# Optimization experiments

Hardware: AMD Instinct MI355X
Metric: run time of the kernel (lower is better)

The kernel has to match this reference:

```python
import jax, jax.numpy as jnp
import numpy as np

B_SZ, D_MODEL, H, W = 4, 192, 64, 64
D_STATE, D_CONV, EXPAND = 16, 4, 2
D_INNER = EXPAND * D_MODEL            # 384
DT_RANK = int(np.ceil(D_MODEL / 16))  # 12


def setup_inputs() -> dict:
    key = jax.random.key(0)
    ks = jax.random.split(key, 12)
    s = 0.02
    # dt bias init so softplus(bias) lands in [1e-3, 0.1] (standard Mamba init)
    dt = jnp.exp(jax.random.uniform(ks[9], (D_INNER,)) * (np.log(0.1) - np.log(1e-3)) + np.log(1e-3))
    dt_proj_b = dt + jnp.log(-jnp.expm1(-dt))
    A_log = jnp.log(jnp.tile(jnp.arange(1, D_STATE + 1, dtype=jnp.float32), (D_INNER, 1)))
    return {
        "x": jax.random.normal(ks[0], (B_SZ, D_MODEL, H, W), jnp.float32),
        "guide": jax.random.normal(ks[1], (B_SZ, D_MODEL, H, W), jnp.float32),
        "guide_w": jax.random.normal(ks[2], (D_MODEL, D_MODEL), jnp.float32) * s,
        "ln_g": jnp.ones((D_MODEL,), jnp.float32),
        "ln_b": jnp.zeros((D_MODEL,), jnp.float32),
        "in_proj_w": jax.random.normal(ks[3], (2 * D_INNER, D_MODEL), jnp.float32) * s,
        "conv_w": jax.random.normal(ks[4], (D_INNER, D_CONV), jnp.float32) * 0.1,
        "conv_b": jnp.zeros((D_INNER,), jnp.float32),
        "x_proj_w": jax.random.normal(ks[5], (DT_RANK + 2 * D_STATE, D_INNER), jnp.float32) * s,
        "dt_proj_w": jax.random.normal(ks[6], (D_INNER, DT_RANK), jnp.float32) * s,
        "dt_proj_b": dt_proj_b,
        "A_log": A_log,
        "D": jnp.ones((D_INNER,), jnp.float32),
        "out_proj_w": jax.random.normal(ks[7], (D_MODEL, D_INNER), jnp.float32) * s,
    }


def reference(x, guide, guide_w, ln_g, ln_b, in_proj_w, conv_w, conv_b,
              x_proj_w, dt_proj_w, dt_proj_b, A_log, D, out_proj_w):
    B, C, Hh, Ww = x.shape
    L = Hh * Ww
    # 1x1 guide conv fuse, flatten to raster sequence [B, L, C]
    g = jnp.einsum('oc,bchw->bohw', guide_w, guide)
    seq = (x + g).reshape(B, C, L).transpose(0, 2, 1)
    # pre-norm (LayerNorm over channels)
    mu = seq.mean(-1, keepdims=True)
    var = seq.var(-1, keepdims=True)
    seq = (seq - mu) / jnp.sqrt(var + 1e-5) * ln_g + ln_b
    # Mamba block: in_proj -> (u, z)
    xz = seq @ in_proj_w.T                       # [B, L, 2*Di]
    u, z = jnp.split(xz, 2, axis=-1)
    # depthwise causal conv along L (kernel D_CONV), then SiLU
    dconv = conv_w.shape[1]
    up = jnp.pad(u, ((0, 0), (dconv - 1, 0), (0, 0)))
    u = sum(up[:, k:k + L, :] * conv_w[:, k] for k in range(dconv)) + conv_b
    u = jax.nn.silu(u)
    # input-dependent dt, B, C
    dbc = u @ x_proj_w.T                         # [B, L, dt_rank + 2*N]
    dt_rank = dt_proj_w.shape[1]
    d_state = A_log.shape[1]
    dt_r = dbc[..., :dt_rank]
    Bt = dbc[..., dt_rank:dt_rank + d_state]
    Ct = dbc[..., dt_rank + d_state:]
    dt = jax.nn.softplus(dt_r @ dt_proj_w.T + dt_proj_b)  # [B, L, Di]
    A = -jnp.exp(A_log)                                   # [Di, N]
    # exact ZOH discretization: Abar = exp(dt*A); Bbar = (exp(dt*A)-1)/A * B
    dA = jnp.exp(dt[..., None] * A)                       # [B, L, Di, N]
    dBu = (dA - 1.0) / A * Bt[:, :, None, :] * u[..., None]

    def step(h, inp):
        dA_l, dBu_l, C_l = inp
        h = dA_l * h + dBu_l                              # [B, Di, N]
        y = jnp.einsum('bdn,bn->bd', h, C_l)
        return h, y

    h0 = jnp.zeros((B, u.shape[-1], d_state), u.dtype)
    _, ys = jax.lax.scan(step, h0, (dA.transpose(1, 0, 2, 3),
                                    dBu.transpose(1, 0, 2, 3),
                                    Ct.transpose(1, 0, 2)))
    y = ys.transpose(1, 0, 2) + u * D                     # [B, L, Di]
    y = y * jax.nn.silu(z)
    out = y @ out_proj_w.T                                # [B, L, C]
    return out.transpose(0, 2, 1).reshape(B, C, Hh, Ww)
```

## Files before the change

### kernel.cpp

```cpp
#include <hip/hip_runtime.h>
#include <hip/hip_bf16.h>

#define Bsz 4
#define Cm 192
#define Lseq 4096
#define Din 384
#define Dst 16
#define NCk 128
#define CLk 32

typedef short s8v __attribute__((ext_vector_type(8)));
typedef float f4v __attribute__((ext_vector_type(4)));
typedef unsigned short ushort_t;

__device__ __forceinline__ unsigned int f2bf(float v) {
  unsigned int u = __float_as_uint(v);
  return (u + 0x7FFFu + ((u >> 16) & 1u)) >> 16;
}
__device__ __forceinline__ float bf2f(unsigned int h) {
  return __uint_as_float(h << 16);
}

#define KP 72

template<int K, int NMAX>
__device__ __forceinline__ void mfma_gemm64(
    const ushort_t* __restrict__ Ah, const ushort_t* __restrict__ Al, long arow0,
    const ushort_t* __restrict__ Bh, const ushort_t* __restrict__ Bl, int nbase,
    ushort_t* sAh, ushort_t* sAl, ushort_t* sBh, ushort_t* sBl,
    f4v acc[2][2]) {
  int t = threadIdx.x;
  int lane = t & 63, w = t >> 6;
  int wm = (w & 1) * 32, wn = (w >> 1) * 32;
  int q = lane >> 4, mr = lane & 15;
  for (int c0 = 0; c0 < K; c0 += 64) {
    if (c0) __syncthreads();
#pragma unroll
    for (int rep = 0; rep < 2; rep++) {
      int s = t + rep * 256;
      int row = s >> 3, kseg = (s & 7) * 8;
      long aoff = (arow0 + row) * (long)K + c0 + kseg;
      int doff = row * KP + kseg;
      *(uint4*)(sAh + doff) = *(const uint4*)(Ah + aoff);
      *(uint4*)(sAl + doff) = *(const uint4*)(Al + aoff);
      if (NMAX >= 64 || (nbase + row) < NMAX) {
        long boff = (long)(nbase + row) * K + c0 + kseg;
        *(uint4*)(sBh + doff) = *(const uint4*)(Bh + boff);
        *(uint4*)(sBl + doff) = *(const uint4*)(Bl + boff);
      } else {
        uint4 z = make_uint4(0u, 0u, 0u, 0u);
        *(uint4*)(sBh + doff) = z;
        *(uint4*)(sBl + doff) = z;
      }
    }
    __syncthreads();
#pragma unroll
    for (int k0 = 0; k0 < 64; k0 += 32) {
      s8v ah[2], al[2], bh[2], bl[2];
#pragma unroll
      for (int mt = 0; mt < 2; mt++) {
        int off = (wm + mt * 16 + mr) * KP + k0 + q * 8;
        ah[mt] = *(const s8v*)(sAh + off);
        al[mt] = *(const s8v*)(sAl + off);
      }
#pragma unroll
      for (int nt = 0; nt < 2; nt++) {
        int off = (wn + nt * 16 + mr) * KP + k0 + q * 8;
        bh[nt] = *(const s8v*)(sBh + off);
        bl[nt] = *(const s8v*)(sBl + off);
      }
#pragma unroll
      for (int mt = 0; mt < 2; mt++)
#pragma unroll
        for (int nt = 0; nt < 2; nt++) {
          acc[mt][nt] = __builtin_amdgcn_mfma_f32_16x16x32_bf16(ah[mt], bh[nt], acc[mt][nt], 0, 0, 0);
          acc[mt][nt] = __builtin_amdgcn_mfma_f32_16x16x32_bf16(ah[mt], bl[nt], acc[mt][nt], 0, 0, 0);
          acc[mt][nt] = __builtin_amdgcn_mfma_f32_16x16x32_bf16(al[mt], bh[nt], acc[mt][nt], 0, 0, 0);
        }
    }
  }
}

__global__ void k_wsplit4(const float* __restrict__ gw, const float* __restrict__ ipw,
                          const float* __restrict__ xw, const float* __restrict__ opw,
                          ushort_t* __restrict__ base) {
  int i = blockIdx.x * 256 + threadIdx.x;
  const float* src; ushort_t *dh, *dl; int off;
  if (i < 36864)        { src = gw;  off = i;           dh = base;          dl = base + 36864; }
  else if (i < 184320)  { src = ipw; off = i - 36864;   dh = base + 73728;  dl = base + 221184; }
  else if (i < 201216)  { src = xw;  off = i - 184320;  dh = base + 368640; dl = base + 385536; }
  else if (i < 274944)  { src = opw; off = i - 201216;  dh = base + 402432; dl = base + 476160; }
  else return;
  float v = src[off];
  unsigned int h = f2bf(v);
  dh[off] = (ushort_t)h;
  dl[off] = (ushort_t)f2bf(v - bf2f(h));
}

__global__ void k_pre(const float* __restrict__ x, const float* __restrict__ guide,
                      float* __restrict__ xT, ushort_t* __restrict__ gTh,
                      ushort_t* __restrict__ gTl) {
  __shared__ float sx[64 * 68];
  __shared__ float sg[64 * 68];
  int t = threadIdx.x;
  int l0 = blockIdx.x * 64;
  int c0 = blockIdx.y * 64;
  int b  = blockIdx.z;
#pragma unroll
  for (int ii = 0; ii < 4; ii++) {
    int ci = (t >> 4) + ii * 16;
    int j4 = (t & 15) * 4;
    long src = ((long)(b * 192 + c0 + ci)) * Lseq + l0 + j4;
    *(float4*)(sx + ci * 68 + j4) = *(const float4*)(x + src);
    *(float4*)(sg + ci * 68 + j4) = *(const float4*)(guide + src);
  }
  __syncthreads();
#pragma unroll
  for (int ii = 0; ii < 4; ii++) {
    int li = (t >> 4) + ii * 16;
    int c4 = (t & 15) * 4;
    long dst = ((long)(b * Lseq + l0 + li)) * 192 + c0 + c4;
    float4 xv = make_float4(sx[(c4 + 0) * 68 + li], sx[(c4 + 1) * 68 + li],
                            sx[(c4 + 2) * 68 + li], sx[(c4 + 3) * 68 + li]);
    *(float4*)(xT + dst) = xv;
    float gv[4];
#pragma unroll
    for (int j = 0; j < 4; j++) gv[j] = sg[(c4 + j) * 68 + li];
    ushort4 hv, lv;
    unsigned int h0 = f2bf(gv[0]), h1 = f2bf(gv[1]), h2 = f2bf(gv[2]), h3 = f2bf(gv[3]);
    hv.x = h0; hv.y = h1; hv.z = h2; hv.w = h3;
    lv.x = (ushort_t)f2bf(gv[0] - bf2f(h0));
    lv.y = (ushort_t)f2bf(gv[1] - bf2f(h1));
    lv.z = (ushort_t)f2bf(gv[2] - bf2f(h2));
    lv.w = (ushort_t)f2bf(gv[3] - bf2f(h3));
    *(ushort4*)(gTh + dst) = hv;
    *(ushort4*)(gTl + dst) = lv;
  }
}

__global__ __launch_bounds__(256) void k_guide_mfma(
    const ushort_t* __restrict__ Ah, const ushort_t* __restrict__ Al,
    const ushort_t* __restrict__ Bh, const ushort_t* __restrict__ Bl,
    const float* __restrict__ xT, float* __restrict__ gxT) {
  __shared__ __align__(16) ushort_t smem[4 * 64 * KP];
  ushort_t* sAh = smem;
  ushort_t* sAl = smem + 64 * KP;
  ushort_t* sBh = smem + 2 * 64 * KP;
  ushort_t* sBl = smem + 3 * 64 * KP;
  int t = threadIdx.x;
  int rowbase = blockIdx.x * 64;
  int nbase = blockIdx.y * 64;
  int lane = t & 63, w = t >> 6;
  int wm = (w & 1) * 32, wn = (w >> 1) * 32;
  int q = lane >> 4, mr = lane & 15;
  f4v acc[2][2];
#pragma unroll
  for (int i = 0; i < 2; i++)
#pragma unroll
    for (int j = 0; j < 2; j++) acc[i][j] = (f4v){0.f, 0.f, 0.f, 0.f};
  mfma_gemm64<192, 192>(Ah, Al, rowbase, Bh, Bl, nbase, sAh, sAl, sBh, sBl, acc);
#pragma unroll
  for (int mt = 0; mt < 2; mt++)
#pragma unroll
    for (int nt = 0; nt < 2; nt++) {
      int row = rowbase + wm + mt * 16 + q * 4;
      int col = nbase + wn + nt * 16 + mr;
#pragma unroll
      for (int r = 0; r < 4; r++) {
        long idx = (long)(row + r) * 192 + col;
        gxT[idx] = acc[mt][nt][r] + xT[idx];
      }
    }
}

__global__ void k_lnT(const float* __restrict__ gxT, const float* __restrict__ ln_g,
                      const float* __restrict__ ln_b, ushort_t* __restrict__ seqh,
                      ushort_t* __restrict__ seql) {
  int t = threadIdx.x;
  int r = blockIdx.x * 4 + (t >> 6);
  int lane = t & 63;
  const float* p = gxT + (long)r * 192;
  float v0 = p[lane], v1 = p[lane + 64], v2 = p[lane + 128];
  float sum = v0 + v1 + v2;
  float sq = fmaf(v0, v0, fmaf(v1, v1, v2 * v2));
#pragma unroll
  for (int off = 1; off < 64; off <<= 1) {
    sum += __shfl_xor(sum, off);
    sq  += __shfl_xor(sq, off);
  }
  float mu = sum / 192.f;
  float rstd = rsqrtf(sq / 192.f - mu * mu + 1e-5f);
  long base = (long)r * 192;
#pragma unroll
  for (int j = 0; j < 3; j++) {
    int c = lane + j * 64;
    float v = (p[c] - mu) * rstd * ln_g[c] + ln_b[c];
    unsigned int h = f2bf(v);
    seqh[base + c] = (ushort_t)h;
    seql[base + c] = (ushort_t)f2bf(v - bf2f(h));
  }
}

__global__ __launch_bounds__(256) void k_inproj_mfma(
    const ushort_t* __restrict__ Ah, const ushort_t* __restrict__ Al,
    const ushort_t* __restrict__ Bh, const ushort_t* __restrict__ Bl,
    float* __restrict__ xzu, float* __restrict__ z) {
  __shared__ __align__(16) ushort_t smem[4 * 64 * KP];
  ushort_t* sAh = smem;
  ushort_t* sAl = smem + 64 * KP;
  ushort_t* sBh = smem + 2 * 64 * KP;
  ushort_t* sBl = smem + 3 * 64 * KP;
  int t = threadIdx.x;
  int rowbase = blockIdx.x * 64;
  int nbase = blockIdx.y * 64;
  int lane = t & 63, w = t >> 6;
  int wm = (w & 1) * 32, wn = (w >> 1) * 32;
  int q = lane >> 4, mr = lane & 15;
  f4v acc[2][2];
#pragma unroll
  for (int i = 0; i < 2; i++)
#pragma unroll
    for (int j = 0; j < 2; j++) acc[i][j] = (f4v){0.f, 0.f, 0.f, 0.f};
  mfma_gemm64<192, 768>(Ah, Al, rowbase, Bh, Bl, nbase, sAh, sAl, sBh, sBl, acc);
  float* dst = (nbase < 384) ? xzu : z;
  int cb = (nbase < 384) ? nbase : nbase - 384;
#pragma unroll
  for (int mt = 0; mt < 2; mt++)
#pragma unroll
    for (int nt = 0; nt < 2; nt++) {
      int row = rowbase + wm + mt * 16 + q * 4;
      int col = cb + wn + nt * 16 + mr;
#pragma unroll
      for (int r = 0; r < 4; r++)
        dst[(long)(row + r) * 384 + col] = acc[mt][nt][r];
    }
}

__global__ void k_conv(const float* __restrict__ xzu, const float* __restrict__ cw,
                       const float* __restrict__ cb, float* __restrict__ u,
                       ushort_t* __restrict__ uh, ushort_t* __restrict__ ul) {
  int idx = blockIdx.x * 256 + threadIdx.x;
  if (idx >= Bsz * Lseq * Din) return;
  int d = idx % Din;
  int l = (idx / Din) % Lseq;
  float acc = cb[d];
#pragma unroll
  for (int k = 0; k < 4; k++) {
    int ls = l - 3 + k;
    if (ls >= 0) acc = fmaf(xzu[idx - (3 - k) * 384], cw[d * 4 + k], acc);
  }
  float v = acc / (1.f + __expf(-acc));
  u[idx] = v;
  unsigned int h = f2bf(v);
  uh[idx] = (ushort_t)h;
  ul[idx] = (ushort_t)f2bf(v - bf2f(h));
}

__global__ __launch_bounds__(256) void k_xproj_mfma(
    const ushort_t* __restrict__ Ah, const ushort_t* __restrict__ Al,
    const ushort_t* __restrict__ Bh, const ushort_t* __restrict__ Bl,
    float* __restrict__ dbc) {
  __shared__ __align__(16) ushort_t smem[4 * 64 * KP];
  ushort_t* sAh = smem;
  ushort_t* sAl = smem + 64 * KP;
  ushort_t* sBh = smem + 2 * 64 * KP;
  ushort_t* sBl = smem + 3 * 64 * KP;
  int t = threadIdx.x;
  int rowbase = blockIdx.x * 64;
  int lane = t & 63, w = t >> 6;
  int wm = (w & 1) * 32, wn = (w >> 1) * 32;
  int q = lane >> 4, mr = lane & 15;
  f4v acc[2][2];
#pragma unroll
  for (int i = 0; i < 2; i++)
#pragma unroll
    for (int j = 0; j < 2; j++) acc[i][j] = (f4v){0.f, 0.f, 0.f, 0.f};
  mfma_gemm64<384, 44>(Ah, Al, rowbase, Bh, Bl, 0, sAh, sAl, sBh, sBl, acc);
#pragma unroll
  for (int mt = 0; mt < 2; mt++)
#pragma unroll
    for (int nt = 0; nt < 2; nt++) {
      int row = rowbase + wm + mt * 16 + q * 4;
      int col = wn + nt * 16 + mr;
      if (col < 44) {
#pragma unroll
        for (int r = 0; r < 4; r++)
          dbc[(long)(row + r) * 48 + col] = acc[mt][nt][r];
      }
    }
}

__global__ void k_dtsplit(const float* __restrict__ dbc, const float* __restrict__ dtw,
                          const float* __restrict__ dtb, float* __restrict__ dt,
                          float* __restrict__ Bc, float* __restrict__ Cc) {
  int idx = blockIdx.x * 256 + threadIdx.x;
  int row = idx / 384;
  int d = idx % 384;
  const float* p = dbc + (long)row * 48;
  float acc = dtb[d];
#pragma unroll
  for (int r = 0; r < 12; r++) acc = fmaf(p[r], dtw[d * 12 + r], acc);
  float sp = (acc > 20.f) ? acc : __logf(1.f + __expf(acc));
  dt[(long)row * 384 + d] = sp;
  if (d < 16) Bc[row * 16 + d] = p[12 + d];
  else if (d < 32) Cc[row * 16 + (d - 16)] = p[28 + (d - 16)];
}

__global__ void k_prep(const float* __restrict__ Alog, float* __restrict__ Aexp,
                       float* __restrict__ rAe) {
  int i = blockIdx.x * 256 + threadIdx.x;
  if (i < Din * Dst) {
    float A = -__expf(Alog[i]);
    Aexp[i] = A;
    rAe[i] = 1.f / A;
  }
}

__global__ void k_scanA(const float* __restrict__ dt, const float* __restrict__ u,
                        const float* __restrict__ Bc, const float* __restrict__ Aexp,
                        const float* __restrict__ rAe,
                        float* __restrict__ Ssum, float* __restrict__ Sdt) {
  int d = threadIdx.x;
  int c = blockIdx.x;
  int b = blockIdx.y;
  float A[16], rA[16], h[16];
  const float4* Ap4 = (const float4*)(Aexp + d * 16);
  const float4* Rp4 = (const float4*)(rAe + d * 16);
#pragma unroll
  for (int j = 0; j < 4; j++) {
    float4 av = Ap4[j], rv = Rp4[j];
    A[4 * j + 0] = av.x; A[4 * j + 1] = av.y; A[4 * j + 2] = av.z; A[4 * j + 3] = av.w;
    rA[4 * j + 0] = rv.x; rA[4 * j + 1] = rv.y; rA[4 * j + 2] = rv.z; rA[4 * j + 3] = rv.w;
  }
#pragma unroll
  for (int n = 0; n < 16; n++) h[n] = 0.f;
  float sdt = 0.f;
  long row0 = (long)b * Lseq + (long)c * CLk;
  const float* dtp = dt + row0 * 384 + d;
  const float* up  = u  + row0 * 384 + d;
  const float* Bp  = Bc + row0 * 16;
#pragma unroll 2
  for (int i = 0; i < CLk; i++) {
    float dtv = dtp[i * 384];
    float uv  = up[i * 384];
    float Bv[16];
#pragma unroll
    for (int j = 0; j < 4; j++) {
      float4 bv = *(const float4*)(Bp + i * 16 + j * 4);
      Bv[4 * j + 0] = bv.x; Bv[4 * j + 1] = bv.y; Bv[4 * j + 2] = bv.z; Bv[4 * j + 3] = bv.w;
    }
    sdt += dtv;
#pragma unroll
    for (int n = 0; n < 16; n++) {
      float a = __expf(dtv * A[n]);
      float q = rA[n] * Bv[n] * uv;
      h[n] = fmaf(a, h[n] + q, -q);
    }
  }
  long o = ((long)(b * NCk + c) * 384 + d);
  Sdt[o] = sdt;
#pragma unroll
  for (int j = 0; j < 4; j++) {
    *(float4*)(Ssum + o * 16 + j * 4) = make_float4(h[4*j], h[4*j+1], h[4*j+2], h[4*j+3]);
  }
}

__global__ void k_scanB(const float* __restrict__ Ssum, const float* __restrict__ Sdt,
                        const float* __restrict__ Aexp, float* __restrict__ Hst) {
  int g = blockIdx.x * 256 + threadIdx.x;
  int n = g & 15;
  int d = (g >> 4) % 384;
  int b = g / (384 * 16);
  float A = Aexp[d * 16 + n];
  float h = 0.f;
  for (int c = 0; c < NCk; c++) {
    long o = ((long)(b * NCk + c) * 384 + d);
    float aC = __expf(A * Sdt[o]);
    Hst[o * 16 + n] = h;
    h = fmaf(aC, h, Ssum[o * 16 + n]);
  }
}

__global__ void k_scanC(const float* __restrict__ dt, const float* __restrict__ u,
                        const float* __restrict__ Bc, const float* __restrict__ Cc,
                        const float* __restrict__ Aexp, const float* __restrict__ rAe,
                        const float* __restrict__ Hst, const float* __restrict__ Dp,
                        const float* __restrict__ z, ushort_t* __restrict__ yyh,
                        ushort_t* __restrict__ yyl) {
  int d = threadIdx.x;
  int c = blockIdx.x;
  int b = blockIdx.y;
  float A[16], rA[16], h[16];
  const float4* Ap4 = (const float4*)(Aexp + d * 16);
  const float4* Rp4 = (const float4*)(rAe + d * 16);
#pragma unroll
  for (int j = 0; j < 4; j++) {
    float4 av = Ap4[j], rv = Rp4[j];
    A[4 * j + 0] = av.x; A[4 * j + 1] = av.y; A[4 * j + 2] = av.z; A[4 * j + 3] = av.w;
    rA[4 * j + 0] = rv.x; rA[4 * j + 1] = rv.y; rA[4 * j + 2] = rv.z; rA[4 * j + 3] = rv.w;
  }
  long o = ((long)(b * NCk + c) * 384 + d);
#pragma unroll
  for (int j = 0; j < 4; j++) {
    float4 hv = *(const float4*)(Hst + o * 16 + j * 4);
    h[4 * j + 0] = hv.x; h[4 * j + 1] = hv.y; h[4 * j + 2] = hv.z; h[4 * j + 3] = hv.w;
  }
  float Dv = Dp[d];
  long row0 = (long)b * Lseq + (long)c * CLk;
  const float* dtp = dt + row0 * 384 + d;
  const float* up  = u  + row0 * 384 + d;
  const float* Bp  = Bc + row0 * 16;
  const float* Cp  = Cc + row0 * 16;
  const float* zp  = z + row0 * 384 + d;
#pragma unroll 2
  for (int i = 0; i < CLk; i++) {
    float dtv = dtp[i * 384];
    float uv  = up[i * 384];
    float zv  = zp[i * 384];
    float Bv[16], Cv[16];
#pragma unroll
    for (int j = 0; j < 4; j++) {
      float4 bv = *(const float4*)(Bp + i * 16 + j * 4);
      float4 cv = *(const float4*)(Cp + i * 16 + j * 4);
      Bv[4 * j + 0] = bv.x; Bv[4 * j + 1] = bv.y; Bv[4 * j + 2] = bv.z; Bv[4 * j + 3] = bv.w;
      Cv[4 * j + 0] = cv.x; Cv[4 * j + 1] = cv.y; Cv[4 * j + 2] = cv.z; Cv[4 * j + 3] = cv.w;
    }
    float yacc = 0.f;
#pragma unroll
    for (int n = 0; n < 16; n++) {
      float a = __expf(dtv * A[n]);
      float q = rA[n] * Bv[n] * uv;
      h[n] = fmaf(a, h[n] + q, -q);
      yacc = fmaf(h[n], Cv[n], yacc);
    }
    float sil = zv / (1.f + __expf(-zv));
    float yv = (yacc + uv * Dv) * sil;
    unsigned int hb = f2bf(yv);
    yyh[row0 * 384 + i * 384 + d] = (ushort_t)hb;
    yyl[row0 * 384 + i * 384 + d] = (ushort_t)f2bf(yv - bf2f(hb));
  }
}

__global__ __launch_bounds__(256) void k_outproj_mfma(
    const ushort_t* __restrict__ Ah, const ushort_t* __restrict__ Al,
    const ushort_t* __restrict__ Bh, const ushort_t* __restrict__ Bl,
    float* __restrict__ out) {
  __shared__ __align__(16) ushort_t smem[4 * 64 * KP];
  ushort_t* sAh = smem;
  ushort_t* sAl = smem + 64 * KP;
  ushort_t* sBh = smem + 2 * 64 * KP;
  ushort_t* sBl = smem + 3 * 64 * KP;
  float* sC = (float*)smem;
  int t = threadIdx.x;
  int rowbase = blockIdx.x * 64;
  int nbase = blockIdx.y * 64;
  int lane = t & 63, w = t >> 6;
  int wm = (w & 1) * 32, wn = (w >> 1) * 32;
  int q = lane >> 4, mr = lane & 15;
  f4v acc[2][2];
#pragma unroll
  for (int i = 0; i < 2; i++)
#pragma unroll
    for (int j = 0; j < 2; j++) acc[i][j] = (f4v){0.f, 0.f, 0.f, 0.f};
  mfma_gemm64<384, 192>(Ah, Al, rowbase, Bh, Bl, nbase, sAh, sAl, sBh, sBl, acc);
  __syncthreads();
#pragma unroll
  for (int mt = 0; mt < 2; mt++)
#pragma unroll
    for (int nt = 0; nt < 2; nt++) {
      int rloc = wm + mt * 16 + q * 4;
      int cloc = wn + nt * 16 + mr;
#pragma unroll
      for (int r = 0; r < 4; r++)
        sC[(rloc + r) * 68 + cloc] = acc[mt][nt][r];
    }
  __syncthreads();
  int b = rowbase >> 12;
  int l0 = rowbase & 4095;
  int o = t >> 2;
  int lg = (t & 3) * 16;
  long obase = ((long)(b * 192 + nbase + o)) * Lseq + l0 + lg;
#pragma unroll
  for (int j4 = 0; j4 < 4; j4++) {
    float4 v = make_float4(sC[(lg + j4 * 4 + 0) * 68 + o], sC[(lg + j4 * 4 + 1) * 68 + o],
                           sC[(lg + j4 * 4 + 2) * 68 + o], sC[(lg + j4 * 4 + 3) * 68 + o]);
    *(float4*)(out + obase + j4 * 4) = v;
  }
}

extern "C" void kernel_launch(void* const* d_in, const int* in_sizes, int n_in,
                              void* d_out, int out_size, void* d_ws, size_t ws_size,
                              hipStream_t stream) {
  const float* x    = (const float*)d_in[0];
  const float* guide= (const float*)d_in[1];
  const float* gw   = (const float*)d_in[2];
  const float* ln_g = (const float*)d_in[3];
  const float* ln_b = (const float*)d_in[4];
  const float* ipw  = (const float*)d_in[5];
  const float* cw   = (const float*)d_in[6];
  const float* cb   = (const float*)d_in[7];
  const float* xpw  = (const float*)d_in[8];
  const float* dtw  = (const float*)d_in[9];
  const float* dtb  = (const float*)d_in[10];
  const float* Alog = (const float*)d_in[11];
  const float* Dp   = (const float*)d_in[12];
  const float* opw  = (const float*)d_in[13];
  float* out = (float*)d_out;
  float* ws  = (float*)d_ws;

  float* xT   = ws + 0;
  ushort_t* uh   = (ushort_t*)(ws + 0);
  float* Ssum = ws + 0;
  ushort_t* gTh  = (ushort_t*)(ws + 3145728);
  ushort_t* gTl  = (ushort_t*)(ws + 3145728 + 1572864);
  ushort_t* ul   = (ushort_t*)(ws + 3145728);
  float* Hst  = ws + 3145728;
  float* gxT  = ws + 6291456;
  float* dbc  = ws + 6291456;
  ushort_t* yyh  = (ushort_t*)(ws + 6291456);
  ushort_t* seqh = (ushort_t*)(ws + 9437184);
  ushort_t* seql = (ushort_t*)(ws + 9437184 + 1572864);
  ushort_t* yyl  = (ushort_t*)(ws + 9437184);
  float* z    = ws + 12582912;
  float* xzu  = ws + 18874368;
  float* dt   = ws + 18874368;
  float* u    = ws + 25165824;
  float* Bc_  = ws + 31457280;
  float* Cc_  = ws + 31719424;
  float* Sdt  = ws + 31981568;
  float* Aexp = ws + 32178176;
  float* rAe  = ws + 32184320;
  ushort_t* wsplit = (ushort_t*)(ws + 32190464);
  ushort_t* gwh = wsplit;
  ushort_t* gwl = wsplit + 36864;
  ushort_t* iwh = wsplit + 73728;
  ushort_t* iwl = wsplit + 221184;
  ushort_t* xwh = wsplit + 368640;
  ushort_t* xwl = wsplit + 385536;
  ushort_t* opwh = wsplit + 402432;
  ushort_t* opwl = wsplit + 476160;

  k_prep    <<<24,               256, 0, stream>>>(Alog, Aexp, rAe);
  k_wsplit4 <<<1074,             256, 0, stream>>>(gw, ipw, xpw, opw, wsplit);
  k_pre     <<<dim3(64, 3, 4),   256, 0, stream>>>(x, guide, xT, gTh, gTl);
  k_guide_mfma<<<dim3(256, 3),   256, 0, stream>>>(gTh, gTl, gwh, gwl, xT, gxT);
  k_lnT     <<<4096,             256, 0, stream>>>(gxT, ln_g, ln_b, seqh, seql);
  k_inproj_mfma<<<dim3(256, 12), 256, 0, stream>>>(seqh, seql, iwh, iwl, xzu, z);
  k_conv    <<<24576,            256, 0, stream>>>(xzu, cw, cb, u, uh, ul);
  k_xproj_mfma<<<256,            256, 0, stream>>>(uh, ul, xwh, xwl, dbc);
  k_dtsplit <<<24576,            256, 0, stream>>>(dbc, dtw, dtb, dt, Bc_, Cc_);
  k_scanA   <<<dim3(NCk, Bsz),   384, 0, stream>>>(dt, u, Bc_, Aexp, rAe, Ssum, Sdt);
  k_scanB   <<<96,               256, 0, stream>>>(Ssum, Sdt, Aexp, Hst);
  k_scanC   <<<dim3(NCk, Bsz),   384, 0, stream>>>(dt, u, Bc_, Cc_, Aexp, rAe, Hst, Dp, z, yyh, yyl);
  k_outproj_mfma<<<dim3(256, 3), 256, 0, stream>>>(yyh, yyl, opwh, opwl, out);
}
```

Before: 309.7 us.

## Fuse conv and dt projection into scan kernels, split state across thread pairs

```diff
diff --git a/kernel.cpp b/kernel.cpp
--- a/kernel.cpp
+++ b/kernel.cpp
@@ -237,8 +237,8 @@
 }
 
 __global__ void k_conv(const float* __restrict__ xzu, const float* __restrict__ cw,
-                       const float* __restrict__ cb, float* __restrict__ u,
-                       ushort_t* __restrict__ uh, ushort_t* __restrict__ ul) {
+                       const float* __restrict__ cb, ushort_t* __restrict__ uh,
+                       ushort_t* __restrict__ ul) {
   int idx = blockIdx.x * 256 + threadIdx.x;
   if (idx >= Bsz * Lseq * Din) return;
   int d = idx % Din;
@@ -250,7 +250,6 @@
     if (ls >= 0) acc = fmaf(xzu[idx - (3 - k) * 384], cw[d * 4 + k], acc);
   }
   float v = acc / (1.f + __expf(-acc));
-  u[idx] = v;
   unsigned int h = f2bf(v);
   uh[idx] = (ushort_t)h;
   ul[idx] = (ushort_t)f2bf(v - bf2f(h));
@@ -290,22 +289,6 @@
     }
 }
 
-__global__ void k_dtsplit(const float* __restrict__ dbc, const float* __restrict__ dtw,
-                          const float* __restrict__ dtb, float* __restrict__ dt,
-                          float* __restrict__ Bc, float* __restrict__ Cc) {
-  int idx = blockIdx.x * 256 + threadIdx.x;
-  int row = idx / 384;
-  int d = idx % 384;
-  const float* p = dbc + (long)row * 48;
-  float acc = dtb[d];
-#pragma unroll
-  for (int r = 0; r < 12; r++) acc = fmaf(p[r], dtw[d * 12 + r], acc);
-  float sp = (acc > 20.f) ? acc : __logf(1.f + __expf(acc));
-  dt[(long)row * 384 + d] = sp;
-  if (d < 16) Bc[row * 16 + d] = p[12 + d];
-  else if (d < 32) Cc[row * 16 + (d - 16)] = p[28 + (d - 16)];
-}
-
 __global__ void k_prep(const float* __restrict__ Alog, float* __restrict__ Aexp,
                        float* __restrict__ rAe) {
   int i = blockIdx.x * 256 + threadIdx.x;
@@ -316,53 +299,81 @@
   }
 }
 
-__global__ void k_scanA(const float* __restrict__ dt, const float* __restrict__ u,
-                        const float* __restrict__ Bc, const float* __restrict__ Aexp,
-                        const float* __restrict__ rAe,
-                        float* __restrict__ Ssum, float* __restrict__ Sdt) {
-  int d = threadIdx.x;
-  int c = blockIdx.x;
-  int b = blockIdx.y;
-  float A[16], rA[16], h[16];
-  const float4* Ap4 = (const float4*)(Aexp + d * 16);
-  const float4* Rp4 = (const float4*)(rAe + d * 16);
-#pragma unroll
-  for (int j = 0; j < 4; j++) {
-    float4 av = Ap4[j], rv = Rp4[j];
-    A[4 * j + 0] = av.x; A[4 * j + 1] = av.y; A[4 * j + 2] = av.z; A[4 * j + 3] = av.w;
-    rA[4 * j + 0] = rv.x; rA[4 * j + 1] = rv.y; rA[4 * j + 2] = rv.z; rA[4 * j + 3] = rv.w;
-  }
-#pragma unroll
-  for (int n = 0; n < 16; n++) h[n] = 0.f;
+__device__ __forceinline__ float softplus_f(float x) {
+  return (x > 20.f) ? x : __logf(1.f + __expf(x));
+}
+
+__global__ __launch_bounds__(384) void k_scanA(
+    const float* __restrict__ xzu, const float* __restrict__ dbc,
+    const float* __restrict__ cw, const float* __restrict__ cb,
+    const float* __restrict__ dtw, const float* __restrict__ dtb,
+    const float* __restrict__ Aexp, const float* __restrict__ rAe,
+    float* __restrict__ Ssum, float* __restrict__ Sdt) {
+  int t = threadIdx.x;
+  int dl = t >> 1, half = t & 1;
+  int dg = blockIdx.y;
+  int d = dg * 192 + dl;
+  int c = blockIdx.x, b = blockIdx.z;
+  float A[8], rA[8];
+  {
+    float4 a0 = *(const float4*)(Aexp + d * 16 + half * 8);
+    float4 a1 = *(const float4*)(Aexp + d * 16 + half * 8 + 4);
+    float4 r0 = *(const float4*)(rAe + d * 16 + half * 8);
+    float4 r1 = *(const float4*)(rAe + d * 16 + half * 8 + 4);
+    A[0]=a0.x;A[1]=a0.y;A[2]=a0.z;A[3]=a0.w;A[4]=a1.x;A[5]=a1.y;A[6]=a1.z;A[7]=a1.w;
+    rA[0]=r0.x;rA[1]=r0.y;rA[2]=r0.z;rA[3]=r0.w;rA[4]=r1.x;rA[5]=r1.y;rA[6]=r1.z;rA[7]=r1.w;
+  }
+  float cwd[4];
+#pragma unroll
+  for (int k = 0; k < 4; k++) cwd[k] = cw[d * 4 + k];
+  float cbd = cb[d];
+  float wt[6];
+#pragma unroll
+  for (int r = 0; r < 4; r++) wt[r] = dtw[d * 12 + half * 8 + r];
+  wt[4] = dtw[d * 12 + 4 + half * 2];
+  wt[5] = dtw[d * 12 + 4 + half * 2 + 1];
+  float dtbd = dtb[d];
+  long row0 = (long)b * Lseq + (long)c * CLk;
+  float w1 = 0.f, w2 = 0.f, w3 = 0.f;
+  if (c > 0) {
+    w3 = xzu[(row0 - 3) * 384 + d];
+    w2 = xzu[(row0 - 2) * 384 + d];
+    w1 = xzu[(row0 - 1) * 384 + d];
+  }
+  float h[8];
+#pragma unroll
+  for (int n = 0; n < 8; n++) h[n] = 0.f;
   float sdt = 0.f;
-  long row0 = (long)b * Lseq + (long)c * CLk;
-  const float* dtp = dt + row0 * 384 + d;
-  const float* up  = u  + row0 * 384 + d;
-  const float* Bp  = Bc + row0 * 16;
+  const float* xp = xzu + row0 * 384 + d;
+  const float* dp = dbc + row0 * 48;
 #pragma unroll 2
   for (int i = 0; i < CLk; i++) {
-    float dtv = dtp[i * 384];
-    float uv  = up[i * 384];
-    float Bv[16];
-#pragma unroll
-    for (int j = 0; j < 4; j++) {
-      float4 bv = *(const float4*)(Bp + i * 16 + j * 4);
-      Bv[4 * j + 0] = bv.x; Bv[4 * j + 1] = bv.y; Bv[4 * j + 2] = bv.z; Bv[4 * j + 3] = bv.w;
-    }
+    float x0 = xp[i * 384];
+    float ua = cbd;
+    ua = fmaf(w3, cwd[0], ua); ua = fmaf(w2, cwd[1], ua);
+    ua = fmaf(w1, cwd[2], ua); ua = fmaf(x0, cwd[3], ua);
+    float uv = ua / (1.f + __expf(-ua));
+    w3 = w2; w2 = w1; w1 = x0;
+    float4 qa = *(const float4*)(dp + i * 48 + half * 8);
+    float2 qb = *(const float2*)(dp + i * 48 + 4 + half * 2);
+    float part = qa.x * wt[0] + qa.y * wt[1] + qa.z * wt[2] + qa.w * wt[3]
+               + qb.x * wt[4] + qb.y * wt[5];
+    float dtv = softplus_f(part + __shfl_xor(part, 1) + dtbd);
     sdt += dtv;
-#pragma unroll
-    for (int n = 0; n < 16; n++) {
+    float4 b0 = *(const float4*)(dp + i * 48 + 12 + half * 8);
+    float4 b1 = *(const float4*)(dp + i * 48 + 16 + half * 8);
+    float Bv[8] = {b0.x, b0.y, b0.z, b0.w, b1.x, b1.y, b1.z, b1.w};
+#pragma unroll
+    for (int n = 0; n < 8; n++) {
       float a = __expf(dtv * A[n]);
       float q = rA[n] * Bv[n] * uv;
       h[n] = fmaf(a, h[n] + q, -q);
     }
   }
   long o = ((long)(b * NCk + c) * 384 + d);
-  Sdt[o] = sdt;
-#pragma unroll
-  for (int j = 0; j < 4; j++) {
-    *(float4*)(Ssum + o * 16 + j * 4) = make_float4(h[4*j], h[4*j+1], h[4*j+2], h[4*j+3]);
-  }
+  if (half == 0) Sdt[o] = sdt;
+  *(float4*)(Ssum + o * 16 + half * 8)     = make_float4(h[0], h[1], h[2], h[3]);
+  *(float4*)(Ssum + o * 16 + half * 8 + 4) = make_float4(h[4], h[5], h[6], h[7]);
 }
 
 __global__ void k_scanB(const float* __restrict__ Ssum, const float* __restrict__ Sdt,
@@ -381,63 +392,92 @@
   }
 }
 
-__global__ void k_scanC(const float* __restrict__ dt, const float* __restrict__ u,
-                        const float* __restrict__ Bc, const float* __restrict__ Cc,
-                        const float* __restrict__ Aexp, const float* __restrict__ rAe,
-                        const float* __restrict__ Hst, const float* __restrict__ Dp,
-                        const float* __restrict__ z, ushort_t* __restrict__ yyh,
-                        ushort_t* __restrict__ yyl) {
-  int d = threadIdx.x;
-  int c = blockIdx.x;
-  int b = blockIdx.y;
-  float A[16], rA[16], h[16];
-  const float4* Ap4 = (const float4*)(Aexp + d * 16);
-  const float4* Rp4 = (const float4*)(rAe + d * 16);
-#pragma unroll
-  for (int j = 0; j < 4; j++) {
-    float4 av = Ap4[j], rv = Rp4[j];
-    A[4 * j + 0] = av.x; A[4 * j + 1] = av.y; A[4 * j + 2] = av.z; A[4 * j + 3] = av.w;
-    rA[4 * j + 0] = rv.x; rA[4 * j + 1] = rv.y; rA[4 * j + 2] = rv.z; rA[4 * j + 3] = rv.w;
-  }
+__global__ __launch_bounds__(384) void k_scanC(
+    const float* __restrict__ xzu, const float* __restrict__ dbc,
+    const float* __restrict__ cw, const float* __restrict__ cb,
+    const float* __restrict__ dtw, const float* __restrict__ dtb,
+    const float* __restrict__ Aexp, const float* __restrict__ rAe,
+    const float* __restrict__ Hst, const float* __restrict__ Dp,
+    const float* __restrict__ z, ushort_t* __restrict__ yyh,
+    ushort_t* __restrict__ yyl) {
+  int t = threadIdx.x;
+  int dl = t >> 1, half = t & 1;
+  int dg = blockIdx.y;
+  int d = dg * 192 + dl;
+  int c = blockIdx.x, b = blockIdx.z;
+  float A[8], rA[8];
+  {
+    float4 a0 = *(const float4*)(Aexp + d * 16 + half * 8);
+    float4 a1 = *(const float4*)(Aexp + d * 16 + half * 8 + 4);
+    float4 r0 = *(const float4*)(rAe + d * 16 + half * 8);
+    float4 r1 = *(const float4*)(rAe + d * 16 + half * 8 + 4);
+    A[0]=a0.x;A[1]=a0.y;A[2]=a0.z;A[3]=a0.w;A[4]=a1.x;A[5]=a1.y;A[6]=a1.z;A[7]=a1.w;
+    rA[0]=r0.x;rA[1]=r0.y;rA[2]=r0.z;rA[3]=r0.w;rA[4]=r1.x;rA[5]=r1.y;rA[6]=r1.z;rA[7]=r1.w;
+  }
+  float cwd[4];
+#pragma unroll
+  for (int k = 0; k < 4; k++) cwd[k] = cw[d * 4 + k];
+  float cbd = cb[d];
+  float wt[6];
+#pragma unroll
+  for (int r = 0; r < 4; r++) wt[r] = dtw[d * 12 + half * 8 + r];
+  wt[4] = dtw[d * 12 + 4 + half * 2];
+  wt[5] = dtw[d * 12 + 4 + half * 2 + 1];
+  float dtbd = dtb[d];
+  float Dv = Dp[d];
   long o = ((long)(b * NCk + c) * 384 + d);
-#pragma unroll
-  for (int j = 0; j < 4; j++) {
-    float4 hv = *(const float4*)(Hst + o * 16 + j * 4);
-    h[4 * j + 0] = hv.x; h[4 * j + 1] = hv.y; h[4 * j + 2] = hv.z; h[4 * j + 3] = hv.w;
-  }
-  float Dv = Dp[d];
+  float h[8];
+  {
+    float4 h0 = *(const float4*)(Hst + o * 16 + half * 8);
+    float4 h1 = *(const float4*)(Hst + o * 16 + half * 8 + 4);
+    h[0]=h0.x;h[1]=h0.y;h[2]=h0.z;h[3]=h0.w;h[4]=h1.x;h[5]=h1.y;h[6]=h1.z;h[7]=h1.w;
+  }
   long row0 = (long)b * Lseq + (long)c * CLk;
-  const float* dtp = dt + row0 * 384 + d;
-  const float* up  = u  + row0 * 384 + d;
-  const float* Bp  = Bc + row0 * 16;
-  const float* Cp  = Cc + row0 * 16;
-  const float* zp  = z + row0 * 384 + d;
+  float w1 = 0.f, w2 = 0.f, w3 = 0.f;
+  if (c > 0) {
+    w3 = xzu[(row0 - 3) * 384 + d];
+    w2 = xzu[(row0 - 2) * 384 + d];
+    w1 = xzu[(row0 - 1) * 384 + d];
+  }
+  const float* xp = xzu + row0 * 384 + d;
+  const float* dp = dbc + row0 * 48;
+  const float* zp = z + row0 * 384 + d;
 #pragma unroll 2
   for (int i = 0; i < CLk; i++) {
-    float dtv = dtp[i * 384];
-    float uv  = up[i * 384];
-    float zv  = zp[i * 384];
-    float Bv[16], Cv[16];
-#pragma unroll
-    for (int j = 0; j < 4; j++) {
-      float4 bv = *(const float4*)(Bp + i * 16 + j * 4);
-      float4 cv = *(const float4*)(Cp + i * 16 + j * 4);
-      Bv[4 * j + 0] = bv.x; Bv[4 * j + 1] = bv.y; Bv[4 * j + 2] = bv.z; Bv[4 * j + 3] = bv.w;
-      Cv[4 * j + 0] = cv.x; Cv[4 * j + 1] = cv.y; Cv[4 * j + 2] = cv.z; Cv[4 * j + 3] = cv.w;
-    }
+    float x0 = xp[i * 384];
+    float ua = cbd;
+    ua = fmaf(w3, cwd[0], ua); ua = fmaf(w2, cwd[1], ua);
+    ua = fmaf(w1, cwd[2], ua); ua = fmaf(x0, cwd[3], ua);
+    float uv = ua / (1.f + __expf(-ua));
+    w3 = w2; w2 = w1; w1 = x0;
+    float4 qa = *(const float4*)(dp + i * 48 + half * 8);
+    float2 qb = *(const float2*)(dp + i * 48 + 4 + half * 2);
+    float part = qa.x * wt[0] + qa.y * wt[1] + qa.z * wt[2] + qa.w * wt[3]
+               + qb.x * wt[4] + qb.y * wt[5];
+    float dtv = softplus_f(part + __shfl_xor(part, 1) + dtbd);
+    float4 b0 = *(const float4*)(dp + i * 48 + 12 + half * 8);
+    float4 b1 = *(const float4*)(dp + i * 48 + 16 + half * 8);
+    float Bv[8] = {b0.x, b0.y, b0.z, b0.w, b1.x, b1.y, b1.z, b1.w};
+    float4 c0v = *(const float4*)(dp + i * 48 + 28 + half * 8);
+    float4 c1v = *(const float4*)(dp + i * 48 + 32 + half * 8);
+    float Cv[8] = {c0v.x, c0v.y, c0v.z, c0v.w, c1v.x, c1v.y, c1v.z, c1v.w};
     float yacc = 0.f;
 #pragma unroll
-    for (int n = 0; n < 16; n++) {
+    for (int n = 0; n < 8; n++) {
       float a = __expf(dtv * A[n]);
       float q = rA[n] * Bv[n] * uv;
       h[n] = fmaf(a, h[n] + q, -q);
       yacc = fmaf(h[n], Cv[n], yacc);
     }
-    float sil = zv / (1.f + __expf(-zv));
-    float yv = (yacc + uv * Dv) * sil;
-    unsigned int hb = f2bf(yv);
-    yyh[row0 * 384 + i * 384 + d] = (ushort_t)hb;
-    yyl[row0 * 384 + i * 384 + d] = (ushort_t)f2bf(yv - bf2f(hb));
+    float ytot = yacc + __shfl_xor(yacc, 1);
+    if (half == 0) {
+      float zv = zp[i * 384];
+      float sil = zv / (1.f + __expf(-zv));
+      float yv = (ytot + uv * Dv) * sil;
+      unsigned int hb = f2bf(yv);
+      yyh[row0 * 384 + i * 384 + d] = (ushort_t)hb;
+      yyl[row0 * 384 + i * 384 + d] = (ushort_t)f2bf(yv - bf2f(hb));
+    }
   }
 }
 
@@ -511,22 +551,18 @@
   float* xT   = ws + 0;
   ushort_t* uh   = (ushort_t*)(ws + 0);
   float* Ssum = ws + 0;
+  ushort_t* yyh  = (ushort_t*)(ws + 0);
   ushort_t* gTh  = (ushort_t*)(ws + 3145728);
   ushort_t* gTl  = (ushort_t*)(ws + 3145728 + 1572864);
   ushort_t* ul   = (ushort_t*)(ws + 3145728);
   float* Hst  = ws + 3145728;
   float* gxT  = ws + 6291456;
   float* dbc  = ws + 6291456;
-  ushort_t* yyh  = (ushort_t*)(ws + 6291456);
   ushort_t* seqh = (ushort_t*)(ws + 9437184);
   ushort_t* seql = (ushort_t*)(ws + 9437184 + 1572864);
   ushort_t* yyl  = (ushort_t*)(ws + 9437184);
   float* z    = ws + 12582912;
   float* xzu  = ws + 18874368;
-  float* dt   = ws + 18874368;
-  float* u    = ws + 25165824;
-  float* Bc_  = ws + 31457280;
-  float* Cc_  = ws + 31719424;
   float* Sdt  = ws + 31981568;
   float* Aexp = ws + 32178176;
   float* rAe  = ws + 32184320;
@@ -546,11 +582,10 @@
   k_guide_mfma<<<dim3(256, 3),   256, 0, stream>>>(gTh, gTl, gwh, gwl, xT, gxT);
   k_lnT     <<<4096,             256, 0, stream>>>(gxT, ln_g, ln_b, seqh, seql);
   k_inproj_mfma<<<dim3(256, 12), 256, 0, stream>>>(seqh, seql, iwh, iwl, xzu, z);
-  k_conv    <<<24576,            256, 0, stream>>>(xzu, cw, cb, u, uh, ul);
+  k_conv    <<<24576,            256, 0, stream>>>(xzu, cw, cb, uh, ul);
   k_xproj_mfma<<<256,            256, 0, stream>>>(uh, ul, xwh, xwl, dbc);
-  k_dtsplit <<<24576,            256, 0, stream>>>(dbc, dtw, dtb, dt, Bc_, Cc_);
-  k_scanA   <<<dim3(NCk, Bsz),   384, 0, stream>>>(dt, u, Bc_, Aexp, rAe, Ssum, Sdt);
+  k_scanA   <<<dim3(NCk, 2, Bsz), 384, 0, stream>>>(xzu, dbc, cw, cb, dtw, dtb, Aexp, rAe, Ssum, Sdt);
   k_scanB   <<<96,               256, 0, stream>>>(Ssum, Sdt, Aexp, Hst);
-  k_scanC   <<<dim3(NCk, Bsz),   384, 0, stream>>>(dt, u, Bc_, Cc_, Aexp, rAe, Hst, Dp, z, yyh, yyl);
+  k_scanC   <<<dim3(NCk, 2, Bsz), 384, 0, stream>>>(xzu, dbc, cw, cb, dtw, dtb, Aexp, rAe, Hst, Dp, z, yyh, yyl);
   k_outproj_mfma<<<dim3(256, 3), 256, 0, stream>>>(yyh, yyl, opwh, opwl, out);
 }
```

Measured after the change: 342.2 us. +10.5%, slower.
